# Kernel optimization log

Hardware: AMD Instinct MI355X
Metric: run time of the kernel (lower is better)

The kernel has to match this reference:

```python
import jax, jax.numpy as jnp
import numpy as np

E = 8       # num experts
D = 768     # embed_dim
H = 12      # num heads
F = 3072    # expert hidden = 4*D
TOPK = 2


def setup_inputs() -> dict:
    key = jax.random.key(0)
    ks = jax.random.split(key, 8)
    B, S = 4, 1024
    s = lambda d: 1.0 / np.sqrt(d)
    return {
        "x": jax.random.normal(ks[0], (B, S, D), jnp.float32),
        "w_qkv": jax.random.normal(ks[1], (D, 3 * D), jnp.float32) * s(D),
        "b_qkv": jnp.zeros((3 * D,), jnp.float32),
        "w_o": jax.random.normal(ks[2], (D, D), jnp.float32) * s(D),
        "b_o": jnp.zeros((D,), jnp.float32),
        "w_router": jax.random.normal(ks[3], (D, E), jnp.float32) * s(D),
        "w1": jax.random.normal(ks[4], (E, D, F), jnp.float32) * s(D),
        "b1": jnp.zeros((E, F), jnp.float32),
        "w2": jax.random.normal(ks[5], (E, F, D), jnp.float32) * s(F),
        "b2": jnp.zeros((E, D), jnp.float32),
    }


def reference(x, w_qkv, b_qkv, w_o, b_o, w_router, w1, b1, w2, b2):
    B, S, Dm = x.shape
    hd = Dm // H
    # --- multi-head self-attention ---
    qkv = x @ w_qkv + b_qkv                                  # [B,S,3D]
    q, k, v = jnp.split(qkv, 3, axis=-1)
    resh = lambda t: t.reshape(B, S, H, hd).transpose(0, 2, 1, 3)  # [B,H,S,hd]
    q, k, v = resh(q), resh(k), resh(v)
    scores = jnp.einsum('bhqd,bhkd->bhqk', q, k) / np.sqrt(hd).astype(np.float32)
    attn = jax.nn.softmax(scores, axis=-1)
    ctx = jnp.einsum('bhqk,bhkd->bhqd', attn, v)
    ctx = ctx.transpose(0, 2, 1, 3).reshape(B, S, Dm)
    y = ctx @ w_o + b_o                                      # [B,S,D]
    # --- top-k MoE feed-forward ---
    t = y.reshape(B * S, Dm)                                 # [T,D]
    logits = t @ w_router                                    # [T,E]
    probs = jax.nn.softmax(logits, axis=-1)
    topv, topi = jax.lax.top_k(probs, TOPK)                  # [T,K]
    topw = topv / jnp.sum(topv, axis=-1, keepdims=True)      # renormalized gates
    T = t.shape[0]
    wfull = jnp.zeros_like(probs).at[jnp.arange(T)[:, None], topi].set(topw)  # [T,E]
    # dense all-expert compute, weighted combine (faithful to routed math)
    h = jax.nn.gelu(jnp.einsum('td,edf->etf', t, w1) + b1[:, None, :])  # [E,T,F]
    oe = jnp.einsum('etf,efd->etd', h, w2) + b2[:, None, :]              # [E,T,D]
    out = jnp.einsum('te,etd->td', wfull, oe).reshape(B, S, Dm)
    diagnostics = probs  # router probabilities as diagnostics
    return (out, diagnostics)
```

## Files before the change

kernel.cpp:

```cpp
#include <hip/hip_runtime.h>
#include <hip/hip_bf16.h>
#include <cstdint>
#include <cmath>

#define T_TOK 4096
#define DIM   768
#define HEADS 12
#define HD    64
#define NEXP  8
#define FDIM  3072

typedef __attribute__((ext_vector_type(8))) short short8v;
typedef __attribute__((ext_vector_type(4))) float float4v;

__device__ __forceinline__ float gelu_tanh(float x) {
  float u = 0.7978845608028654f * (x + 0.044715f * x * x * x);
  return 0.5f * x * (1.0f + tanhf(u));
}

__device__ __forceinline__ short f2bf(float x) {
  __hip_bfloat16 h = __float2bfloat16(x);
  return *reinterpret_cast<short*>(&h);
}

__device__ __forceinline__ void gld16(void* lds, const void* g) {
  __builtin_amdgcn_global_load_lds(
      (__attribute__((address_space(1))) void*)(uintptr_t)g,
      (__attribute__((address_space(3))) void*)(uint32_t)(uintptr_t)lds,
      16, 0, 0);
}

template<int TBM, int TBN, bool BFOUT>
__global__ __launch_bounds__(256) void gemm_f32(
    const float* __restrict__ A, const float* __restrict__ W,
    const float* __restrict__ bias, float* __restrict__ C,
    short* __restrict__ Cbf, int M, int N, int K)
{
  constexpr int MM = TBM / 16;
  constexpr int MN = TBN / 16;
  constexpr int AL4 = TBM / 64;
  constexpr int BL4 = TBN / 64;
  __shared__ float As[16][TBM + 4];
  __shared__ float Bs[16][TBN + 4];
  const int bm = blockIdx.y * TBM;
  const int bn = blockIdx.x * TBN;
  const int tid = threadIdx.x;
  const int tr = tid >> 4;
  const int tc = tid & 15;

  float acc[MM][MN] = {};

  for (int k0 = 0; k0 < K; k0 += 16) {
    #pragma unroll
    for (int i = 0; i < AL4; i++) {
      int fidx = tid + i * 256;
      int row = fidx >> 2, c4 = fidx & 3;
      float4 v = *(const float4*)&A[(size_t)(bm + row) * K + k0 + c4 * 4];
      As[c4 * 4 + 0][row] = v.x;
      As[c4 * 4 + 1][row] = v.y;
      As[c4 * 4 + 2][row] = v.z;
      As[c4 * 4 + 3][row] = v.w;
    }
    #pragma unroll
    for (int i = 0; i < BL4; i++) {
      int fidx = tid + i * 256;
      int kk = fidx / (TBN / 4), n4 = fidx % (TBN / 4);
      *(float4*)&Bs[kk][n4 * 4] =
          *(const float4*)&W[(size_t)(k0 + kk) * N + bn + n4 * 4];
    }
    __syncthreads();
    #pragma unroll
    for (int kk = 0; kk < 16; kk++) {
      float a[MM], b[MN];
      #pragma unroll
      for (int u4 = 0; u4 < MM / 4; u4++) {
        float4 t = *(const float4*)&As[kk][tr * MM + u4 * 4];
        a[u4*4+0]=t.x; a[u4*4+1]=t.y; a[u4*4+2]=t.z; a[u4*4+3]=t.w;
      }
      #pragma unroll
      for (int v4 = 0; v4 < MN / 4; v4++) {
        float4 t = *(const float4*)&Bs[kk][tc * MN + v4 * 4];
        b[v4*4+0]=t.x; b[v4*4+1]=t.y; b[v4*4+2]=t.z; b[v4*4+3]=t.w;
      }
      #pragma unroll
      for (int u = 0; u < MM; u++)
        #pragma unroll
        for (int v = 0; v < MN; v++)
          acc[u][v] = fmaf(a[u], b[v], acc[u][v]);
    }
    __syncthreads();
  }

  #pragma unroll
  for (int u = 0; u < MM; u++) {
    int row = bm + tr * MM + u;
    #pragma unroll
    for (int v4 = 0; v4 < MN / 4; v4++) {
      int col = bn + tc * MN + v4 * 4;
      float4 o;
      o.x = acc[u][v4*4+0] + bias[col+0];
      o.y = acc[u][v4*4+1] + bias[col+1];
      o.z = acc[u][v4*4+2] + bias[col+2];
      o.w = acc[u][v4*4+3] + bias[col+3];
      *(float4*)&C[(size_t)row * N + col] = o;
      if (BFOUT) {
        short4 s = make_short4(f2bf(o.x), f2bf(o.y), f2bf(o.z), f2bf(o.w));
        *(short4*)&Cbf[(size_t)row * N + col] = s;
      }
    }
  }
}

__global__ __launch_bounds__(256) void transpose_bf16(
    const float* __restrict__ W, short* __restrict__ WT, int K, int N)
{
  __shared__ float t[32][33];
  const size_t mat = (size_t)K * N;
  const float* Wp = W + blockIdx.z * mat;
  short* WTp = WT + blockIdx.z * mat;
  int n0 = blockIdx.x * 32, k0 = blockIdx.y * 32;
  int tx = threadIdx.x, ty = threadIdx.y;
  #pragma unroll
  for (int i = 0; i < 4; i++)
    t[ty + i * 8][tx] = Wp[(size_t)(k0 + ty + i * 8) * N + n0 + tx];
  __syncthreads();
  #pragma unroll
  for (int i = 0; i < 4; i++)
    WTp[(size_t)(n0 + ty + i * 8) * K + k0 + tx] = f2bf(t[tx][ty + i * 8]);
}

template<int MODE>
__global__ __launch_bounds__(256) void moe_mm(
    const short* __restrict__ A, const short* __restrict__ WT,
    const float* __restrict__ bias, void* __restrict__ Cout,
    int N, int K,
    const int* __restrict__ offsets, const int* __restrict__ perm,
    const int* __restrict__ tmap, const int* __restrict__ tilecnt)
{
  const int bx = blockIdx.x;
  if (bx >= tilecnt[0]) return;
  const int info  = tmap[bx];
  const int e     = info >> 16;
  const int start = offsets[e];
  const int M     = offsets[e + 1] - start;
  const int bm    = (info & 0xffff) * 128;
  const int bn    = blockIdx.y * 128;

  __shared__ short As[8][128][8];
  __shared__ short Bs[8][128][8];
  __shared__ int   perm_s[128];

  const int tid  = threadIdx.x;
  const int lane = tid & 63;
  const int wave = tid >> 6;
  const int wm = wave >> 1, wn = wave & 1;
  const int lr = lane & 15;
  const int kb = lane >> 4;

  const short* WTe = WT + (size_t)e * ((size_t)N * K);
  const float* be  = bias + (size_t)e * N;

  if (MODE == 1) {
    if (tid < 128) {
      int rr = bm + tid;
      perm_s[tid] = (rr < M) ? perm[start + rr] : perm[start];
    }
    __syncthreads();
  }

  const short* asrc0;
  const short* asrc1;
  if (MODE == 1) {
    asrc0 = A + (size_t)perm_s[lane] * K + wave * 8;
    asrc1 = A + (size_t)perm_s[64 + lane] * K + wave * 8;
  } else {
    int r0 = bm + lane;      if (r0 >= M) r0 = M - 1;
    int r1 = bm + 64 + lane; if (r1 >= M) r1 = M - 1;
    asrc0 = A + (size_t)(start + r0) * K + wave * 8;
    asrc1 = A + (size_t)(start + r1) * K + wave * 8;
  }
  const short* bsrc0 = WTe + (size_t)(bn + lane) * K + wave * 8;
  const short* bsrc1 = WTe + (size_t)(bn + 64 + lane) * K + wave * 8;

  float4v acc[4][4] = {};

  for (int k0 = 0; k0 < K; k0 += 64) {
    __syncthreads();
    gld16(&As[wave][0][0],  asrc0 + k0);
    gld16(&As[wave][64][0], asrc1 + k0);
    gld16(&Bs[wave][0][0],  bsrc0 + k0);
    gld16(&Bs[wave][64][0], bsrc1 + k0);
    gld16(&As[wave + 4][0][0],  asrc0 + k0 + 32);
    gld16(&As[wave + 4][64][0], asrc1 + k0 + 32);
    gld16(&Bs[wave + 4][0][0],  bsrc0 + k0 + 32);
    gld16(&Bs[wave + 4][64][0], bsrc1 + k0 + 32);
    __syncthreads();

    #pragma unroll
    for (int hh = 0; hh < 2; hh++) {
      short8v af[4], bfv[4];
      #pragma unroll
      for (int mi = 0; mi < 4; mi++)
        af[mi] = *(const short8v*)&As[hh * 4 + kb][wm * 64 + mi * 16 + lr][0];
      #pragma unroll
      for (int ni = 0; ni < 4; ni++)
        bfv[ni] = *(const short8v*)&Bs[hh * 4 + kb][wn * 64 + ni * 16 + lr][0];
      #pragma unroll
      for (int mi = 0; mi < 4; mi++)
        #pragma unroll
        for (int ni = 0; ni < 4; ni++)
          acc[mi][ni] = __builtin_amdgcn_mfma_f32_16x16x32_bf16(
              af[mi], bfv[ni], acc[mi][ni], 0, 0, 0);
    }
  }

  #pragma unroll
  for (int ni = 0; ni < 4; ni++) {
    int col = bn + wn * 64 + ni * 16 + lr;
    float b = be[col];
    #pragma unroll
    for (int mi = 0; mi < 4; mi++) {
      int lrow0 = wm * 64 + mi * 16 + kb * 4;
      #pragma unroll
      for (int r = 0; r < 4; r++) {
        int rr = bm + lrow0 + r;
        if (rr < M) {
          if (MODE == 1) {
            short* C = (short*)Cout;
            C[(size_t)(start + rr) * N + col] = f2bf(gelu_tanh(acc[mi][ni][r] + b));
          } else {
            float* C = (float*)Cout;
            C[(size_t)(start + rr) * N + col] = acc[mi][ni][r] + b;
          }
        }
      }
    }
  }
}

__global__ __launch_bounds__(256) void combine_kernel(
    const float* __restrict__ oe, const int* __restrict__ ppos,
    const float* __restrict__ topg, float* __restrict__ out)
{
  int g = blockIdx.x * 256 + threadIdx.x;
  int t = g / 192;
  int c = (g - t * 192) * 4;
  int p0 = ppos[2 * t], p1 = ppos[2 * t + 1];
  float g0 = topg[2 * t], g1 = topg[2 * t + 1];
  float4 a = *(const float4*)&oe[(size_t)p0 * DIM + c];
  float4 b = *(const float4*)&oe[(size_t)p1 * DIM + c];
  float4 o;
  o.x = g0 * a.x + g1 * b.x;
  o.y = g0 * a.y + g1 * b.y;
  o.z = g0 * a.z + g1 * b.z;
  o.w = g0 * a.w + g1 * b.w;
  *(float4*)&out[(size_t)t * DIM + c] = o;
}

__global__ __launch_bounds__(512) void attn_kernel(
    const float* __restrict__ qkv, float* __restrict__ ctx)
{
  const int qt = blockIdx.x;
  const int bh = blockIdx.y;
  const int b = bh / HEADS, h = bh % HEADS;
  const float* base = qkv + (size_t)b * 1024 * (3 * DIM) + h * 64;

  __shared__ float ks[64 * 64];
  __shared__ float vs[64 * 64];
  __shared__ float lred[2][2][32];

  const int tid   = threadIdx.x;
  const int wv    = tid >> 6;
  const int qhalf = wv & 1;
  const int kq    = wv >> 1;
  const int lane  = tid & 63;
  const int grp   = lane >> 2;
  const int sub   = lane & 3;
  const int q0    = qhalf * 32 + grp * 2;
  const int dpart = sub * 16;

  const float qscale = 0.125f * 1.44269504088896f;
  float qA[16], qB[16], accA[16] = {}, accB[16] = {};
  float lA = 0.f, lB = 0.f;

  {
    const float* qpA = base + (size_t)(qt * 64 + q0) * (3 * DIM) + dpart;
    const float* qpB = qpA + 3 * DIM;
    #pragma unroll
    for (int d4 = 0; d4 < 4; d4++) {
      float4 ta = *(const float4*)(qpA + d4 * 4);
      float4 tb = *(const float4*)(qpB + d4 * 4);
      qA[d4*4+0]=ta.x*qscale; qA[d4*4+1]=ta.y*qscale; qA[d4*4+2]=ta.z*qscale; qA[d4*4+3]=ta.w*qscale;
      qB[d4*4+0]=tb.x*qscale; qB[d4*4+1]=tb.y*qscale; qB[d4*4+2]=tb.z*qscale; qB[d4*4+3]=tb.w*qscale;
    }
  }

  for (int kt = 0; kt < 16; kt++) {
    __syncthreads();
    #pragma unroll
    for (int i = 0; i < 2; i++) {
      int idx = tid + i * 512;
      int r = idx >> 4, c4 = idx & 15;
      const float* kp = base + (size_t)(kt * 64 + r) * (3 * DIM) + c4 * 4;
      *(float4*)&ks[r * 64 + c4 * 4] = *(const float4*)(kp + DIM);
      *(float4*)&vs[r * 64 + c4 * 4] = *(const float4*)(kp + 2 * DIM);
    }
    __syncthreads();

    #pragma unroll 2
    for (int jj = 0; jj < 16; jj++) {
      int j = kq * 16 + jj;
      float4 k0v = *(const float4*)&ks[j * 64 + dpart];
      float4 k1v = *(const float4*)&ks[j * 64 + dpart + 4];
      float4 k2v = *(const float4*)&ks[j * 64 + dpart + 8];
      float4 k3v = *(const float4*)&ks[j * 64 + dpart + 12];
      float kr[16] = {k0v.x,k0v.y,k0v.z,k0v.w, k1v.x,k1v.y,k1v.z,k1v.w,
                      k2v.x,k2v.y,k2v.z,k2v.w, k3v.x,k3v.y,k3v.z,k3v.w};
      float sA = 0.f, sB = 0.f;
      #pragma unroll
      for (int d = 0; d < 16; d++) {
        sA = fmaf(qA[d], kr[d], sA);
        sB = fmaf(qB[d], kr[d], sB);
      }
      sA += __shfl_xor(sA, 1);  sB += __shfl_xor(sB, 1);
      sA += __shfl_xor(sA, 2);  sB += __shfl_xor(sB, 2);
      float pA = exp2f(sA);
      float pB = exp2f(sB);
      lA += pA;  lB += pB;
      float4 v0v = *(const float4*)&vs[j * 64 + dpart];
      float4 v1v = *(const float4*)&vs[j * 64 + dpart + 4];
      float4 v2v = *(const float4*)&vs[j * 64 + dpart + 8];
      float4 v3v = *(const float4*)&vs[j * 64 + dpart + 12];
      float vr[16] = {v0v.x,v0v.y,v0v.z,v0v.w, v1v.x,v1v.y,v1v.z,v1v.w,
                      v2v.x,v2v.y,v2v.z,v2v.w, v3v.x,v3v.y,v3v.z,v3v.w};
      #pragma unroll
      for (int d = 0; d < 16; d++) {
        accA[d] = fmaf(pA, vr[d], accA[d]);
        accB[d] = fmaf(pB, vr[d], accB[d]);
      }
    }
  }

  float* regA = ks + qhalf * 2048;
  float* regB = vs + qhalf * 2048;
  const int r0 = (grp * 2) * 64 + dpart;
  const int r1 = r0 + 64;

  __syncthreads();
  if (kq == 2 || kq == 3) {
    float* buf = (kq == 2) ? regA : regB;
    #pragma unroll
    for (int d4 = 0; d4 < 4; d4++) {
      *(float4*)&buf[r0 + d4*4] =
          make_float4(accA[d4*4], accA[d4*4+1], accA[d4*4+2], accA[d4*4+3]);
      *(float4*)&buf[r1 + d4*4] =
          make_float4(accB[d4*4], accB[d4*4+1], accB[d4*4+2], accB[d4*4+3]);
    }
    if (sub == 0) {
      lred[kq - 2][qhalf][grp * 2]     = lA;
      lred[kq - 2][qhalf][grp * 2 + 1] = lB;
    }
  }
  __syncthreads();
  if (kq == 0 || kq == 1) {
    const float* buf = (kq == 0) ? regA : regB;
    #pragma unroll
    for (int d4 = 0; d4 < 4; d4++) {
      float4 a = *(const float4*)&buf[r0 + d4*4];
      float4 c = *(const float4*)&buf[r1 + d4*4];
      accA[d4*4+0] += a.x; accA[d4*4+1] += a.y; accA[d4*4+2] += a.z; accA[d4*4+3] += a.w;
      accB[d4*4+0] += c.x; accB[d4*4+1] += c.y; accB[d4*4+2] += c.z; accB[d4*4+3] += c.w;
    }
    lA += lred[kq][qhalf][grp * 2];
    lB += lred[kq][qhalf][grp * 2 + 1];
  }
  __syncthreads();
  if (kq == 1) {
    #pragma unroll
    for (int d4 = 0; d4 < 4; d4++) {
      *(float4*)&regA[r0 + d4*4] =
          make_float4(accA[d4*4], accA[d4*4+1], accA[d4*4+2], accA[d4*4+3]);
      *(float4*)&regA[r1 + d4*4] =
          make_float4(accB[d4*4], accB[d4*4+1], accB[d4*4+2], accB[d4*4+3]);
    }
    if (sub == 0) {
      lred[0][qhalf][grp * 2]     = lA;
      lred[0][qhalf][grp * 2 + 1] = lB;
    }
  }
  __syncthreads();
  if (kq == 0) {
    #pragma unroll
    for (int d4 = 0; d4 < 4; d4++) {
      float4 a = *(const float4*)&regA[r0 + d4*4];
      float4 c = *(const float4*)&regA[r1 + d4*4];
      accA[d4*4+0] += a.x; accA[d4*4+1] += a.y; accA[d4*4+2] += a.z; accA[d4*4+3] += a.w;
      accB[d4*4+0] += c.x; accB[d4*4+1] += c.y; accB[d4*4+2] += c.z; accB[d4*4+3] += c.w;
    }
    lA += lred[0][qhalf][grp * 2];
    lB += lred[0][qhalf][grp * 2 + 1];
    float invA = 1.f / lA, invB = 1.f / lB;
    float* opA = ctx + ((size_t)b * 1024 + qt * 64 + q0) * DIM + h * 64 + dpart;
    float* opB = opA + DIM;
    #pragma unroll
    for (int d4 = 0; d4 < 4; d4++) {
      float4 oa, ob;
      oa.x = accA[d4*4+0]*invA; oa.y = accA[d4*4+1]*invA;
      oa.z = accA[d4*4+2]*invA; oa.w = accA[d4*4+3]*invA;
      ob.x = accB[d4*4+0]*invB; ob.y = accB[d4*4+1]*invB;
      ob.z = accB[d4*4+2]*invB; ob.w = accB[d4*4+3]*invB;
      *(float4*)(opA + d4 * 4) = oa;
      *(float4*)(opB + d4 * 4) = ob;
    }
  }
}

__global__ __launch_bounds__(256) void router_kernel(
    const float* __restrict__ y, const float* __restrict__ wr,
    float* __restrict__ probs, int* __restrict__ topi,
    float* __restrict__ topg, int* __restrict__ counts)
{
  __shared__ float w[DIM * NEXP];
  const int tid = threadIdx.x;
  for (int i = tid; i < DIM * NEXP; i += 256) w[i] = wr[i];
  __syncthreads();

  const int t = blockIdx.x * 256 + tid;
  const float* yp = y + (size_t)t * DIM;
  float logit[8] = {};
  for (int d = 0; d < DIM; d++) {
    float xv = yp[d];
    #pragma unroll
    for (int e = 0; e < 8; e++) logit[e] = fmaf(xv, w[d * 8 + e], logit[e]);
  }
  float mx = logit[0];
  #pragma unroll
  for (int e = 1; e < 8; e++) mx = fmaxf(mx, logit[e]);
  float p[8], sum = 0.f;
  #pragma unroll
  for (int e = 0; e < 8; e++) { p[e] = __expf(logit[e] - mx); sum += p[e]; }
  float inv = 1.f / sum;
  #pragma unroll
  for (int e = 0; e < 8; e++) { p[e] *= inv; probs[(size_t)t * 8 + e] = p[e]; }

  int i0 = 0;
  #pragma unroll
  for (int e = 1; e < 8; e++) if (p[e] > p[i0]) i0 = e;
  int i1 = (i0 == 0) ? 1 : 0;
  #pragma unroll
  for (int e = 0; e < 8; e++) if (e != i0 && p[e] > p[i1]) i1 = e;
  float g = p[i0] + p[i1];
  topi[2 * t] = i0;  topi[2 * t + 1] = i1;
  topg[2 * t] = p[i0] / g;  topg[2 * t + 1] = p[i1] / g;
  atomicAdd(&counts[i0], 1);
  atomicAdd(&counts[i1], 1);
}

__global__ void init_meta(int* counts) {
  if (threadIdx.x < 8) counts[threadIdx.x] = 0;
}

__global__ void scan_kernel(const int* __restrict__ counts,
                            int* __restrict__ offsets, int* __restrict__ cursors,
                            int* __restrict__ tmap, int* __restrict__ tilecnt) {
  if (threadIdx.x == 0) {
    int s = 0;
    for (int e = 0; e < 8; e++) { offsets[e] = s; cursors[e] = s; s += counts[e]; }
    offsets[8] = s;
    int tu = 0;
    for (int e = 0; e < 8; e++) {
      int m = counts[e];
      for (int t = 0; t * 128 < m; t++) tmap[tu++] = (e << 16) | t;
    }
    tilecnt[0] = tu;
  }
}

__global__ __launch_bounds__(256) void scatter_kernel(
    const int* __restrict__ topi, int* __restrict__ cursors,
    int* __restrict__ perm, int* __restrict__ ppos)
{
  const int t = blockIdx.x * 256 + threadIdx.x;
  #pragma unroll
  for (int s = 0; s < 2; s++) {
    int e = topi[2 * t + s];
    int pos = atomicAdd(&cursors[e], 1);
    perm[pos] = t;
    ppos[2 * t + s] = pos;
  }
}

extern "C" void kernel_launch(void* const* d_in, const int* in_sizes, int n_in,
                              void* d_out, int out_size, void* d_ws, size_t ws_size,
                              hipStream_t stream) {
  const float* x        = (const float*)d_in[0];
  const float* w_qkv    = (const float*)d_in[1];
  const float* b_qkv    = (const float*)d_in[2];
  const float* w_o      = (const float*)d_in[3];
  const float* b_o      = (const float*)d_in[4];
  const float* w_router = (const float*)d_in[5];
  const float* w1       = (const float*)d_in[6];
  const float* b1       = (const float*)d_in[7];
  const float* w2       = (const float*)d_in[8];
  const float* b2       = (const float*)d_in[9];

  float* out   = (float*)d_out;
  float* probs = out + (size_t)T_TOK * DIM;

  char* ws = (char*)d_ws;
  float* qkv  = (float*)ws;
  short* hbuf = (short*)ws;
  short* wT   = (short*)(ws + 50331648);
  float* ctx  = (float*)(ws + 88080384);
  float* oe   = (float*)(ws + 88080384);
  float* y    = (float*)(ws + 100663296);
  short* ybf  = (short*)(ws + 113246208);
  char*  meta = ws + 119537664;
  int*   counts  = (int*)meta;
  int*   cursors = counts + 8;
  int*   offsets = cursors + 8;
  int*   topi    = offsets + 16;
  float* topg    = (float*)(topi + 8192);
  int*   perm    = (int*)(topg + 8192);
  int*   ppos    = perm + 8192;
  int*   tmap    = ppos + 8192;
  int*   tilecnt = tmap + 80;

  init_meta<<<1, 64, 0, stream>>>(counts);

  gemm_f32<128, 128, false><<<dim3((3 * DIM) / 128, T_TOK / 128), 256, 0, stream>>>(
      x, w_qkv, b_qkv, qkv, nullptr, T_TOK, 3 * DIM, DIM);

  attn_kernel<<<dim3(16, 48), 512, 0, stream>>>(qkv, ctx);

  gemm_f32<64, 64, true><<<dim3(DIM / 64, T_TOK / 64), 256, 0, stream>>>(
      ctx, w_o, b_o, y, ybf, T_TOK, DIM, DIM);

  router_kernel<<<16, 256, 0, stream>>>(y, w_router, probs, topi, topg, counts);
  scan_kernel<<<1, 64, 0, stream>>>(counts, offsets, cursors, tmap, tilecnt);
  scatter_kernel<<<16, 256, 0, stream>>>(topi, cursors, perm, ppos);

  transpose_bf16<<<dim3(FDIM / 32, DIM / 32, NEXP), dim3(32, 8), 0, stream>>>(
      w1, wT, DIM, FDIM);
  moe_mm<1><<<dim3(72, FDIM / 128), 256, 0, stream>>>(
      ybf, wT, b1, hbuf, FDIM, DIM, offsets, perm, tmap, tilecnt);

  transpose_bf16<<<dim3(DIM / 32, FDIM / 32, NEXP), dim3(32, 8), 0, stream>>>(
      w2, wT, FDIM, DIM);
  moe_mm<2><<<dim3(72, DIM / 128), 256, 0, stream>>>(
      hbuf, wT, b2, oe, DIM, FDIM, offsets, perm, tmap, tilecnt);

  combine_kernel<<<(T_TOK * DIM / 4) / 256, 256, 0, stream>>>(oe, ppos, topg, out);
}
```

Measured before the change: 976.2 us.

## Split-K the second MoE expert GEMM and use a cheaper sigmoid-form GELU

The down-projection MoE GEMM (K=3072, N=768) only had 72x6 blocks. It is now split along K into two halves written to separate fp32 buffers, and the combine kernel sums the partials before applying the gates. This is meant to raise occupancy on the many CUs. In exchange it costs an extra 25 MB write and read, and it only takes effect if the workspace is large enough. Separately, the tanh-based GELU is rewritten as an exact equivalent x*sigmoid(2u) using exp2 and a fast reciprocal, which lowers epilogue cost.

```diff
diff --git a/kernel.cpp b/kernel.cpp
--- a/kernel.cpp
+++ b/kernel.cpp
@@ -14,8 +14,9 @@
 typedef __attribute__((ext_vector_type(4))) float float4v;
 
 __device__ __forceinline__ float gelu_tanh(float x) {
-  float u = 0.7978845608028654f * (x + 0.044715f * x * x * x);
-  return 0.5f * x * (1.0f + tanhf(u));
+  float u = x + 0.044715f * x * x * x;
+  float e = exp2f(-2.302236563f * u);
+  return x * __builtin_amdgcn_rcpf(1.0f + e);
 }
 
 __device__ __forceinline__ short f2bf(float x) {
@@ -133,7 +134,7 @@
 __global__ __launch_bounds__(256) void moe_mm(
     const short* __restrict__ A, const short* __restrict__ WT,
     const float* __restrict__ bias, void* __restrict__ Cout,
-    int N, int K,
+    void* __restrict__ Cout2, int N, int K, int kdiv,
     const int* __restrict__ offsets, const int* __restrict__ perm,
     const int* __restrict__ tmap, const int* __restrict__ tilecnt)
 {
@@ -145,6 +146,9 @@
   const int M     = offsets[e + 1] - start;
   const int bm    = (info & 0xffff) * 128;
   const int bn    = blockIdx.y * 128;
+  const int kz    = (MODE == 2) ? blockIdx.z : 0;
+  const int Keff  = K / kdiv;
+  const int kbeg  = kz * Keff;
 
   __shared__ short As[8][128][8];
   __shared__ short Bs[8][128][8];
@@ -176,15 +180,15 @@
   } else {
     int r0 = bm + lane;      if (r0 >= M) r0 = M - 1;
     int r1 = bm + 64 + lane; if (r1 >= M) r1 = M - 1;
-    asrc0 = A + (size_t)(start + r0) * K + wave * 8;
-    asrc1 = A + (size_t)(start + r1) * K + wave * 8;
-  }
-  const short* bsrc0 = WTe + (size_t)(bn + lane) * K + wave * 8;
-  const short* bsrc1 = WTe + (size_t)(bn + 64 + lane) * K + wave * 8;
+    asrc0 = A + (size_t)(start + r0) * K + kbeg + wave * 8;
+    asrc1 = A + (size_t)(start + r1) * K + kbeg + wave * 8;
+  }
+  const short* bsrc0 = WTe + (size_t)(bn + lane) * K + kbeg + wave * 8;
+  const short* bsrc1 = WTe + (size_t)(bn + 64 + lane) * K + kbeg + wave * 8;
 
   float4v acc[4][4] = {};
 
-  for (int k0 = 0; k0 < K; k0 += 64) {
+  for (int k0 = 0; k0 < Keff; k0 += 64) {
     __syncthreads();
     gld16(&As[wave][0][0],  asrc0 + k0);
     gld16(&As[wave][64][0], asrc1 + k0);
@@ -217,7 +221,7 @@
   #pragma unroll
   for (int ni = 0; ni < 4; ni++) {
     int col = bn + wn * 64 + ni * 16 + lr;
-    float b = be[col];
+    float b = (kz == 0) ? be[col] : 0.f;
     #pragma unroll
     for (int mi = 0; mi < 4; mi++) {
       int lrow0 = wm * 64 + mi * 16 + kb * 4;
@@ -229,7 +233,7 @@
             short* C = (short*)Cout;
             C[(size_t)(start + rr) * N + col] = f2bf(gelu_tanh(acc[mi][ni][r] + b));
           } else {
-            float* C = (float*)Cout;
+            float* C = (kz == 0) ? (float*)Cout : (float*)Cout2;
             C[(size_t)(start + rr) * N + col] = acc[mi][ni][r] + b;
           }
         }
@@ -238,17 +242,25 @@
   }
 }
 
+template<int KS>
 __global__ __launch_bounds__(256) void combine_kernel(
-    const float* __restrict__ oe, const int* __restrict__ ppos,
-    const float* __restrict__ topg, float* __restrict__ out)
+    const float* __restrict__ oe0, const float* __restrict__ oe1,
+    const int* __restrict__ ppos, const float* __restrict__ topg,
+    float* __restrict__ out)
 {
   int g = blockIdx.x * 256 + threadIdx.x;
   int t = g / 192;
   int c = (g - t * 192) * 4;
   int p0 = ppos[2 * t], p1 = ppos[2 * t + 1];
   float g0 = topg[2 * t], g1 = topg[2 * t + 1];
-  float4 a = *(const float4*)&oe[(size_t)p0 * DIM + c];
-  float4 b = *(const float4*)&oe[(size_t)p1 * DIM + c];
+  float4 a = *(const float4*)&oe0[(size_t)p0 * DIM + c];
+  float4 b = *(const float4*)&oe0[(size_t)p1 * DIM + c];
+  if (KS == 2) {
+    float4 a1 = *(const float4*)&oe1[(size_t)p0 * DIM + c];
+    float4 b1 = *(const float4*)&oe1[(size_t)p1 * DIM + c];
+    a.x += a1.x; a.y += a1.y; a.z += a1.z; a.w += a1.w;
+    b.x += b1.x; b.y += b1.y; b.z += b1.z; b.w += b1.w;
+  }
   float4 o;
   o.x = g0 * a.x + g1 * b.x;
   o.y = g0 * a.y + g1 * b.y;
@@ -512,7 +524,7 @@
   short* hbuf = (short*)ws;
   short* wT   = (short*)(ws + 50331648);
   float* ctx  = (float*)(ws + 88080384);
-  float* oe   = (float*)(ws + 88080384);
+  float* oe0  = (float*)(ws + 88080384);
   float* y    = (float*)(ws + 100663296);
   short* ybf  = (short*)(ws + 113246208);
   char*  meta = ws + 119537664;
@@ -525,6 +537,8 @@
   int*   ppos    = perm + 8192;
   int*   tmap    = ppos + 8192;
   int*   tilecnt = tmap + 80;
+  float* oe1 = (float*)(ws + 119799808);
+  const bool ksplit = (ws_size >= 119799808ull + 25165824ull);
 
   init_meta<<<1, 64, 0, stream>>>(counts);
 
@@ -543,12 +557,20 @@
   transpose_bf16<<<dim3(FDIM / 32, DIM / 32, NEXP), dim3(32, 8), 0, stream>>>(
       w1, wT, DIM, FDIM);
   moe_mm<1><<<dim3(72, FDIM / 128), 256, 0, stream>>>(
-      ybf, wT, b1, hbuf, FDIM, DIM, offsets, perm, tmap, tilecnt);
+      ybf, wT, b1, hbuf, nullptr, FDIM, DIM, 1, offsets, perm, tmap, tilecnt);
 
   transpose_bf16<<<dim3(DIM / 32, FDIM / 32, NEXP), dim3(32, 8), 0, stream>>>(
       w2, wT, FDIM, DIM);
-  moe_mm<2><<<dim3(72, DIM / 128), 256, 0, stream>>>(
-      hbuf, wT, b2, oe, DIM, FDIM, offsets, perm, tmap, tilecnt);
-
-  combine_kernel<<<(T_TOK * DIM / 4) / 256, 256, 0, stream>>>(oe, ppos, topg, out);
-}
+
+  if (ksplit) {
+    moe_mm<2><<<dim3(72, DIM / 128, 2), 256, 0, stream>>>(
+        hbuf, wT, b2, oe0, oe1, DIM, FDIM, 2, offsets, perm, tmap, tilecnt);
+    combine_kernel<2><<<(T_TOK * DIM / 4) / 256, 256, 0, stream>>>(
+        oe0, oe1, ppos, topg, out);
+  } else {
+    moe_mm<2><<<dim3(72, DIM / 128, 1), 256, 0, stream>>>(
+        hbuf, wT, b2, oe0, nullptr, DIM, FDIM, 1, offsets, perm, tmap, tilecnt);
+    combine_kernel<1><<<(T_TOK * DIM / 4) / 256, 256, 0, stream>>>(
+        oe0, nullptr, ppos, topg, out);
+  }
+}
```

Measured after the change: 995.9 us, median of 2. +2.0%, slower.
